# Kernel optimization log

Measured on AMD Instinct MI355X. Metric: run time of the kernel, lower is better.

## Reference

```python
import jax, jax.numpy as jnp
import numpy as np

B, C, H, W = 8, 48, 256, 256
N_PROMPTS = 16
N_EXPERTS = 8
N_GROUPS = 4
TOP_K = 2
GROUP_DIM = C // N_GROUPS
DN = ('NCHW', 'OIHW', 'NCHW')


def _conv(x, w, groups=1, pad=0):
    return jax.lax.conv_general_dilated(
        x, w, window_strides=(1, 1), padding=[(pad, pad), (pad, pad)],
        dimension_numbers=DN, feature_group_count=groups)


def setup_inputs() -> dict:
    key = jax.random.key(0)
    ks = jax.random.split(key, 10)
    s = 0.02
    return {
        'x': jax.random.normal(ks[0], (B, C, H, W), jnp.float32),
        'P_hat': jax.random.normal(ks[1], (B, N_PROMPTS, C), jnp.float32),
        'proj_a_w': jax.random.normal(ks[2], (C, C, 1, 1), jnp.float32) * s,
        'proj_b_w': jax.random.normal(ks[3], (C, C, 1, 1), jnp.float32) * s,
        'dw_b_w': jax.random.normal(ks[4], (C, 1, 3, 3), jnp.float32) * s,
        'fi_align_w': jax.random.normal(ks[5], (C, N_GROUPS, 1, 1), jnp.float32) * s,
        'expert_w1': jax.random.normal(ks[6], (N_EXPERTS, C, C, 3, 3), jnp.float32) * s,
        'expert_w2': jax.random.normal(ks[7], (N_EXPERTS, C, C, 3, 3), jnp.float32) * s,
        'router_w': jax.random.normal(ks[8], (N_EXPERTS, C), jnp.float32) * s,
        'router_b': jax.random.normal(ks[9], (N_EXPERTS,), jnp.float32) * s,
    }


def reference(x, P_hat, proj_a_w, proj_b_w, dw_b_w, fi_align_w,
              expert_w1, expert_w2, router_w, router_b):
    b, c, h, w = x.shape
    # branch a: 1x1 proj + group-wise prompt-conditioned filter activation
    xa = _conv(x, proj_a_w)                               # [B,C,H,W]
    p_avg = P_hat.mean(axis=1)                            # [B,C]
    xa_g = xa.reshape(b, N_GROUPS, GROUP_DIM, h * w)      # [B,G,gd,HW]
    p_g = p_avg.reshape(b, N_GROUPS, GROUP_DIM)           # [B,G,gd]
    fi = jnp.einsum('bgc,bgcn->bgn', p_g, xa_g)           # [B,G,HW]
    fi = fi.reshape(b, N_GROUPS, h, w)
    fi = _conv(fi, fi_align_w)                            # [B,C,H,W]
    # branch b: 1x1 proj + depthwise 3x3
    xb = _conv(_conv(x, proj_b_w), dw_b_w, groups=c, pad=1)
    Fx = xb + fi
    # routing: GAP -> linear -> top-k softmax gate
    gap = Fx.mean(axis=(2, 3))                            # [B,C]
    scores = gap @ router_w.T + router_b                  # [B,E]
    topk_val, topk_idx = jax.lax.top_k(scores, TOP_K)
    gate = jnp.zeros_like(scores).at[
        jnp.arange(b)[:, None], topk_idx
    ].set(jax.nn.softmax(topk_val, axis=-1))              # [B,E]
    # experts: dense compute then weighted sum (matches dense-then-mask math)
    out = jnp.zeros_like(Fx)
    for i in range(N_EXPERTS):
        hmid = jax.nn.gelu(_conv(Fx, expert_w1[i], pad=1), approximate=False)
        e_out = _conv(hmid, expert_w2[i], pad=1)
        out = out + gate[:, i][:, None, None, None] * e_out
    return out + x
```

## Files before the change

### kernel.cpp

```cpp
#include <hip/hip_runtime.h>
#include <hip/hip_bf16.h>
#include <math.h>

#define BATCH 8
#define CH 48
#define HH 256
#define WW 256
#define NPROMPT 16
#define NEXP 8
#define NGRP 4
#define GDIM 12
#define HW (HH * WW)

#define FRAG_ELEMS (9 * 3 * 2 * 64 * 8)
#define FRAG_BYTES (FRAG_ELEMS * 2)

typedef short bf16x8 __attribute__((ext_vector_type(8)));
typedef float f32x4  __attribute__((ext_vector_type(4)));
typedef unsigned short u16x4 __attribute__((ext_vector_type(4)));

#define TILE_W 16
#define TILE_H 8
#define ITILE_W 18
#define ITILE_H 10
#define NPIX (ITILE_W * ITILE_H)
#define PIXB 128
#define ROWB (ITILE_W * PIXB)
#define STAGE_K 23
#define LDSBYTES (STAGE_K * 1024)
#define GPIXB 96
#define IMGB ((size_t)HW * GPIXB)
#define NTILES 512

__device__ __forceinline__ unsigned short f2bf(float f) {
    unsigned u = __float_as_uint(f);
    unsigned r = (u + 0x7FFFu + ((u >> 16) & 1u)) >> 16;
    return (unsigned short)r;
}

__device__ __forceinline__ void load_lds16(const void* g, void* l) {
    __builtin_amdgcn_global_load_lds(
        (const __attribute__((address_space(1))) unsigned int*)g,
        (__attribute__((address_space(3))) unsigned int*)l, 16, 0, 0);
}

__global__ __launch_bounds__(256) void precompute_kernel(
    const float* __restrict__ P_hat,
    const float* __restrict__ proj_a_w,
    const float* __restrict__ proj_b_w,
    const float* __restrict__ dw_b_w,
    const float* __restrict__ fi_align_w,
    unsigned short* __restrict__ wfxf,
    float* __restrict__ zpage)
{
    int b = blockIdx.x;
    int tid = threadIdx.x;
    __shared__ float p_avg[CH];
    __shared__ float W_fi[NGRP * CH];
    __shared__ float W_a[CH * CH];

    if (tid < CH) {
        float s = 0.f;
        for (int n = 0; n < NPROMPT; n++)
            s += P_hat[(b * NPROMPT + n) * CH + tid];
        p_avg[tid] = s * (1.0f / NPROMPT);
    }
    if (b == 0 && tid < 64) zpage[tid] = 0.f;
    __syncthreads();

    if (tid < NGRP * CH) {
        int g = tid / CH, k = tid % CH;
        float s = 0.f;
        for (int j = 0; j < GDIM; j++) {
            int c = g * GDIM + j;
            s += p_avg[c] * proj_a_w[c * CH + k];
        }
        W_fi[tid] = s;
    }
    __syncthreads();

    for (int e = tid; e < CH * CH; e += 256) {
        int o = e / CH, k = e % CH;
        float s = 0.f;
        for (int g = 0; g < NGRP; g++)
            s += fi_align_w[o * NGRP + g] * W_fi[g * CH + k];
        W_a[e] = s;
    }
    __syncthreads();

    for (int i = tid; i < FRAG_ELEMS; i += 256) {
        int j = i & 7;
        int lane = (i >> 3) & 63;
        int blk = i >> 9;
        int kb = blk & 1;
        int tmp = blk >> 1;
        int mt = tmp % 3, tap = tmp / 3;
        int oc = mt * 16 + (lane & 15);
        int cin = kb * 32 + (lane >> 4) * 8 + j;
        float v = 0.f;
        if (cin < CH) {
            v = dw_b_w[oc * 9 + tap] * proj_b_w[oc * CH + cin];
            if (tap == 4) v += W_a[oc * CH + cin];
        }
        wfxf[(size_t)b * FRAG_ELEMS + i] = f2bf(v);
    }
}

__global__ __launch_bounds__(256) void repack_kernel(
    const float* __restrict__ w1, const float* __restrict__ w2,
    unsigned short* __restrict__ w1f, unsigned short* __restrict__ w2f)
{
    int e = blockIdx.x;
    const float* src = blockIdx.y ? w2 : w1;
    unsigned short* dst = blockIdx.y ? w2f : w1f;
    for (int i = threadIdx.x; i < FRAG_ELEMS; i += 256) {
        int j = i & 7;
        int lane = (i >> 3) & 63;
        int blk = i >> 9;
        int kb = blk & 1;
        int tmp = blk >> 1;
        int mt = tmp % 3, tap = tmp / 3;
        int oc = mt * 16 + (lane & 15);
        int cin = kb * 32 + (lane >> 4) * 8 + j;
        float v = (cin < CH) ? src[(((size_t)e * CH + oc) * CH + cin) * 9 + tap] : 0.f;
        dst[(size_t)e * FRAG_ELEMS + i] = f2bf(v);
    }
}

__global__ __launch_bounds__(256) void transpose_kernel(
    const float* __restrict__ x, unsigned short* __restrict__ xT)
{
    __shared__ float t[CH * 65];
    int pix0 = blockIdx.x * 64;
    int b = pix0 >> 16;
    int rem = pix0 & 65535;
    int tid = threadIdx.x;
    int px = tid & 63, c0 = tid >> 6;

    float v[12];
#pragma unroll
    for (int k = 0; k < 12; k++)
        v[k] = x[(((size_t)(b * CH + c0 + 4 * k)) << 16) + rem + px];
#pragma unroll
    for (int k = 0; k < 12; k++)
        t[(c0 + 4 * k) * 65 + px] = v[k];
    __syncthreads();

#pragma unroll
    for (int k = 0; k < 2; k++) {
        int w = tid + 256 * k;
        if (w < 384) {
            int p2 = w / 6, o = w % 6;
            bf16x8 pk;
#pragma unroll
            for (int j = 0; j < 8; j++)
                pk[j] = (short)f2bf(t[(o * 8 + j) * 65 + p2]);
            *(bf16x8*)((char*)xT + (size_t)pix0 * GPIXB + (size_t)w * 16) = pk;
        }
    }
}

__device__ __forceinline__ void stage_swz(
    const char* __restrict__ srcimg, int oy0, int ox0,
    char* smem, const char* __restrict__ zp)
{
    int wv = threadIdx.x >> 6, lane = threadIdx.x & 63;
    for (int k = wv; k < STAGE_K; k += 4) {
        int w = k * 64 + lane;
        int px = w >> 3, o = w & 7;
        int yy = px / ITILE_W, xx = px - yy * ITILE_W;
        int gy = oy0 + yy - 1, gx = ox0 + xx - 1;
        int m = o ^ (gx & 7);
        const char* g = zp;
        if (px < NPIX && (unsigned)gy < 256u && (unsigned)gx < 256u && m < 6)
            g = srcimg + (size_t)((gy << 8) + gx) * GPIXB + m * 16;
        load_lds16(g, smem + k * 1024);
    }
}

template <bool ACC, bool SWAP>
__device__ __forceinline__ void conv_core(
    const char* smem, const unsigned short* __restrict__ wfrag,
    int ox0, f32x4 acc[2][3])
{
    const int lane = threadIdx.x & 63;
    const int wv = threadIdx.x >> 6;
    const int n = lane & 15;
    const int quad = lane >> 4;
    const bf16x8* wp = (const bf16x8*)wfrag;

    if (!ACC) {
#pragma unroll
        for (int g = 0; g < 2; ++g)
#pragma unroll
            for (int mt = 0; mt < 3; ++mt)
                acc[g][mt] = (f32x4){0.f, 0.f, 0.f, 0.f};
    }

    int colb0[3], colb1[3];
#pragma unroll
    for (int dx = 0; dx < 3; ++dx) {
        int key = (ox0 - 1 + dx + n) & 7;
        colb0[dx] = (dx + n) * PIXB + ((quad ^ key) * 16);
        colb1[dx] = (dx + n) * PIXB + (((quad + 4) ^ key) * 16);
    }

    bf16x8 a[2][6];
#pragma unroll
    for (int mt = 0; mt < 3; ++mt) {
        a[0][mt]     = wp[(mt * 2 + 0) * 64 + lane];
        a[0][mt + 3] = wp[(mt * 2 + 1) * 64 + lane];
    }

#pragma unroll
    for (int tap = 0; tap < 9; ++tap) {
        const int cur = tap & 1;
        if (tap < 8) {
#pragma unroll
            for (int mt = 0; mt < 3; ++mt) {
                a[cur ^ 1][mt]     = wp[(((tap + 1) * 3 + mt) * 2 + 0) * 64 + lane];
                a[cur ^ 1][mt + 3] = wp[(((tap + 1) * 3 + mt) * 2 + 1) * 64 + lane];
            }
        }
        const int dy = tap / 3, dx = tap % 3;
#pragma unroll
        for (int g = 0; g < 2; ++g) {
            const int rowb = (wv * 2 + g + dy) * ROWB;
            bf16x8 b0 = *(const bf16x8*)(smem + rowb + colb0[dx]);
            bf16x8 b1 = *(const bf16x8*)(smem + rowb + colb1[dx]);
            if (SWAP) {
                acc[g][0] = __builtin_amdgcn_mfma_f32_16x16x32_bf16(b0, a[cur][0], acc[g][0], 0, 0, 0);
                acc[g][1] = __builtin_amdgcn_mfma_f32_16x16x32_bf16(b0, a[cur][1], acc[g][1], 0, 0, 0);
                acc[g][2] = __builtin_amdgcn_mfma_f32_16x16x32_bf16(b0, a[cur][2], acc[g][2], 0, 0, 0);
                acc[g][0] = __builtin_amdgcn_mfma_f32_16x16x32_bf16(b1, a[cur][3], acc[g][0], 0, 0, 0);
                acc[g][1] = __builtin_amdgcn_mfma_f32_16x16x32_bf16(b1, a[cur][4], acc[g][1], 0, 0, 0);
                acc[g][2] = __builtin_amdgcn_mfma_f32_16x16x32_bf16(b1, a[cur][5], acc[g][2], 0, 0, 0);
            } else {
                acc[g][0] = __builtin_amdgcn_mfma_f32_16x16x32_bf16(a[cur][0], b0, acc[g][0], 0, 0, 0);
                acc[g][1] = __builtin_amdgcn_mfma_f32_16x16x32_bf16(a[cur][1], b0, acc[g][1], 0, 0, 0);
                acc[g][2] = __builtin_amdgcn_mfma_f32_16x16x32_bf16(a[cur][2], b0, acc[g][2], 0, 0, 0);
                acc[g][0] = __builtin_amdgcn_mfma_f32_16x16x32_bf16(a[cur][3], b1, acc[g][0], 0, 0, 0);
                acc[g][1] = __builtin_amdgcn_mfma_f32_16x16x32_bf16(a[cur][4], b1, acc[g][1], 0, 0, 0);
                acc[g][2] = __builtin_amdgcn_mfma_f32_16x16x32_bf16(a[cur][5], b1, acc[g][2], 0, 0, 0);
            }
        }
    }
}

__device__ __forceinline__ void store_pix(
    char* __restrict__ dstimg, int row, int col, int quad,
    const f32x4 v[3])
{
    size_t pb = (size_t)((row << 8) + col) * GPIXB;
#pragma unroll
    for (int mt = 0; mt < 3; ++mt) {
        u16x4 pk;
#pragma unroll
        for (int r = 0; r < 4; ++r) pk[r] = f2bf(v[mt][r]);
        *(u16x4*)(dstimg + pb + mt * 32 + quad * 8) = pk;
    }
}

__global__ __launch_bounds__(256, 4) void fxconv_kernel(
    const unsigned short* __restrict__ xT, const unsigned short* __restrict__ wfxf,
    unsigned short* __restrict__ Fx, float* __restrict__ gapP,
    const float* __restrict__ zp)
{
    __shared__ __align__(16) char smem[LDSBYTES];
    int ox0 = blockIdx.x * TILE_W, oy0 = blockIdx.y * TILE_H, b = blockIdx.z;

    stage_swz((const char*)xT + (size_t)b * IMGB, oy0, ox0, smem, (const char*)zp);
    __syncthreads();

    f32x4 acc[2][3];
    conv_core<false, false>(smem, wfxf + (size_t)b * FRAG_ELEMS, ox0, acc);

    const int lane = threadIdx.x & 63;
    const int wv = threadIdx.x >> 6;
    const int n = lane & 15, quad = lane >> 4;
    char* dimg = (char*)Fx + (size_t)b * IMGB;

    float gsum[3][4];
#pragma unroll
    for (int mt = 0; mt < 3; ++mt)
#pragma unroll
        for (int r = 0; r < 4; ++r) gsum[mt][r] = 0.f;

#pragma unroll
    for (int g = 0; g < 2; ++g) {
        int row = oy0 + wv * 2 + g;
        store_pix(dimg, row, ox0 + n, quad, acc[g]);
#pragma unroll
        for (int mt = 0; mt < 3; ++mt)
#pragma unroll
            for (int r = 0; r < 4; ++r) gsum[mt][r] += acc[g][mt][r];
    }
#pragma unroll
    for (int mt = 0; mt < 3; ++mt)
#pragma unroll
        for (int r = 0; r < 4; ++r) {
            float v = gsum[mt][r];
            v += __shfl_xor(v, 1);
            v += __shfl_xor(v, 2);
            v += __shfl_xor(v, 4);
            v += __shfl_xor(v, 8);
            gsum[mt][r] = v;
        }

    __syncthreads();
    float* smemf = (float*)smem;
    if (n == 0) {
#pragma unroll
        for (int mt = 0; mt < 3; ++mt)
#pragma unroll
            for (int r = 0; r < 4; ++r)
                smemf[wv * CH + mt * 16 + quad * 4 + r] = gsum[mt][r];
    }
    __syncthreads();
    int t = threadIdx.x;
    if (t < CH) {
        float v = smemf[t] + smemf[CH + t] + smemf[2 * CH + t] + smemf[3 * CH + t];
        int tile = blockIdx.y * 16 + blockIdx.x;
        gapP[((size_t)b * NTILES + tile) * CH + t] = v;
    }
}

__global__ __launch_bounds__(256) void route_kernel(
    const float* __restrict__ gapP,
    const float* __restrict__ router_w,
    const float* __restrict__ router_b,
    float* __restrict__ gate, int* __restrict__ eidx)
{
    __shared__ float red4[4 * CH];
    __shared__ float scs[NEXP];
    int b = blockIdx.x, t = threadIdx.x;
    int lane = t & 63, wv = t >> 6;

    const float* s1 = gapP + ((size_t)b * NTILES + t) * CH;
    const float* s2 = s1 + 256 * CH;
    float s[CH];
#pragma unroll
    for (int c = 0; c < CH; c++) s[c] = s1[c] + s2[c];
#pragma unroll
    for (int c = 0; c < CH; c++) {
        float v = s[c];
        v += __shfl_xor(v, 1);
        v += __shfl_xor(v, 2);
        v += __shfl_xor(v, 4);
        v += __shfl_xor(v, 8);
        v += __shfl_xor(v, 16);
        v += __shfl_xor(v, 32);
        if (lane == 0) red4[wv * CH + c] = v;
    }
    __syncthreads();

    if (t < NEXP) {
        float sc = router_b[t];
        for (int c = 0; c < CH; c++) {
            float g = (red4[c] + red4[CH + c] + red4[2 * CH + c] + red4[3 * CH + c])
                      * (1.0f / HW);
            sc += g * router_w[t * CH + c];
        }
        scs[t] = sc;
    }
    __syncthreads();

    if (t == 0) {
        float v0 = -1e30f, v1 = -1e30f;
        int i0 = 0, i1 = 0;
        for (int e = 0; e < NEXP; e++) {
            float se = scs[e];
            if (se > v0) { v1 = v0; i1 = i0; v0 = se; i0 = e; }
            else if (se > v1) { v1 = se; i1 = e; }
        }
        float ex = expf(v1 - v0);
        float dn = 1.0f / (1.0f + ex);
        gate[b * 2 + 0] = dn;
        gate[b * 2 + 1] = ex * dn;
        eidx[b * 2 + 0] = i0;
        eidx[b * 2 + 1] = i1;
    }
}

__global__ __launch_bounds__(256) void scale_kernel(
    const unsigned short* __restrict__ w2f, const float* __restrict__ gate,
    const int* __restrict__ eidx, unsigned short* __restrict__ w2s)
{
    int b = blockIdx.x, s = blockIdx.y;
    int e = eidx[b * 2 + s];
    float g = gate[b * 2 + s];
    const unsigned short* src = w2f + (size_t)e * FRAG_ELEMS;
    unsigned short* dst = w2s + (size_t)(b * 2 + s) * FRAG_ELEMS;
    for (int i = threadIdx.x; i < FRAG_ELEMS; i += 256) {
        float v = __uint_as_float((unsigned)src[i] << 16);
        dst[i] = f2bf(v * g);
    }
}

__global__ __launch_bounds__(256, 4) void conv1_both_kernel(
    const unsigned short* __restrict__ Fx, const unsigned short* __restrict__ w1f,
    const int* __restrict__ eidx, const float* __restrict__ zp,
    unsigned short* __restrict__ hmid0, unsigned short* __restrict__ hmid1)
{
    __shared__ __align__(16) char smem[LDSBYTES];
    int ox0 = blockIdx.x * TILE_W, oy0 = blockIdx.y * TILE_H, b = blockIdx.z;

    stage_swz((const char*)Fx + (size_t)b * IMGB, oy0, ox0, smem, (const char*)zp);
    __syncthreads();

    const int lane = threadIdx.x & 63;
    const int wv = threadIdx.x >> 6;
    const int n = lane & 15, quad = lane >> 4;

    f32x4 acc[2][3];
#pragma unroll
    for (int s = 0; s < 2; ++s) {
        int e = __builtin_amdgcn_readfirstlane(eidx[b * 2 + s]);
        conv_core<false, false>(smem, w1f + (size_t)e * FRAG_ELEMS, ox0, acc);
        char* dimg = (char*)(s ? hmid1 : hmid0) + (size_t)b * IMGB;
#pragma unroll
        for (int g = 0; g < 2; ++g) {
            int row = oy0 + wv * 2 + g;
            f32x4 h[3];
#pragma unroll
            for (int mt = 0; mt < 3; ++mt)
#pragma unroll
                for (int r = 0; r < 4; ++r) {
                    float a = acc[g][mt][r];
                    h[mt][r] = 0.5f * a * (1.0f + erff(a * 0.70710678118654752f));
                }
            store_pix(dimg, row, ox0 + n, quad, h);
        }
    }
}

__global__ __launch_bounds__(256, 4) void conv2_both_kernel(
    const unsigned short* __restrict__ hmid0, const unsigned short* __restrict__ hmid1,
    const unsigned short* __restrict__ w2s, const float* __restrict__ zp,
    const float* __restrict__ x, float* __restrict__ out)
{
    __shared__ __align__(16) char smem[LDSBYTES];
    int d = blockIdx.x;
    int k8   = d & 7;
    int half = (d >> 3) & 1;
    int rest = d >> 4;
    int bx = k8 * 2 + half;
    int by = rest & 31;
    int b  = rest >> 5;
    int ox0 = bx * TILE_W, oy0 = by * TILE_H;

    const int lane = threadIdx.x & 63;
    const int wv = threadIdx.x >> 6;
    const int n = lane & 15, quad = lane >> 4;

    f32x4 xr[2][3];
#pragma unroll
    for (int g = 0; g < 2; ++g) {
        int row = oy0 + wv * 2 + g;
#pragma unroll
        for (int nt = 0; nt < 3; ++nt) {
            int oc = nt * 16 + n;
            size_t idx = (((size_t)b * CH + oc) << 16) + (row << 8) + ox0 + quad * 4;
            xr[g][nt] = *(const f32x4*)(x + idx);
        }
    }

    f32x4 acc[2][3];

    stage_swz((const char*)hmid0 + (size_t)b * IMGB, oy0, ox0, smem, (const char*)zp);
    __syncthreads();
    conv_core<false, true>(smem, w2s + (size_t)(b * 2 + 0) * FRAG_ELEMS, ox0, acc);
    __syncthreads();

    stage_swz((const char*)hmid1 + (size_t)b * IMGB, oy0, ox0, smem, (const char*)zp);
    __syncthreads();
    conv_core<true, true>(smem, w2s + (size_t)(b * 2 + 1) * FRAG_ELEMS, ox0, acc);

#pragma unroll
    for (int g = 0; g < 2; ++g) {
        int row = oy0 + wv * 2 + g;
#pragma unroll
        for (int nt = 0; nt < 3; ++nt) {
            int oc = nt * 16 + n;
            size_t idx = (((size_t)b * CH + oc) << 16) + (row << 8) + ox0 + quad * 4;
            *(f32x4*)(out + idx) = xr[g][nt] + acc[g][nt];
        }
    }
}

extern "C" void kernel_launch(void* const* d_in, const int* in_sizes, int n_in,
                              void* d_out, int out_size, void* d_ws, size_t ws_size,
                              hipStream_t stream) {
    (void)in_sizes; (void)n_in; (void)out_size; (void)ws_size;
    const float* x          = (const float*)d_in[0];
    const float* P_hat      = (const float*)d_in[1];
    const float* proj_a_w   = (const float*)d_in[2];
    const float* proj_b_w   = (const float*)d_in[3];
    const float* dw_b_w     = (const float*)d_in[4];
    const float* fi_align_w = (const float*)d_in[5];
    const float* expert_w1  = (const float*)d_in[6];
    const float* expert_w2  = (const float*)d_in[7];
    const float* router_w   = (const float*)d_in[8];
    const float* router_b   = (const float*)d_in[9];
    float* out = (float*)d_out;

    char* ob = (char*)d_out;
    unsigned short* Fx   = (unsigned short*)ob;
    unsigned short* wfxf = (unsigned short*)(ob + 62914560);
    unsigned short* w1f  = (unsigned short*)(ob + 62914560 + FRAG_BYTES * NEXP);
    unsigned short* w2f  = (unsigned short*)(ob + 62914560 + 2 * FRAG_BYTES * NEXP);
    float*          gapP = (float*)(ob + 64241664);

    char* ws = (char*)d_ws;
    unsigned short* xT    = (unsigned short*)ws;
    unsigned short* hmid1 = (unsigned short*)ws;
    unsigned short* hmid0 = (unsigned short*)(ws + 50331648);
    unsigned short* w2s   = (unsigned short*)(ws + 100663296);
    float* zp   = (float*)(ws + 100663296 + 884736);
    float* gate = (float*)(ws + 100663296 + 884736 + 256 + 1536);
    int*   eidx = (int*)(gate + BATCH * 2);

    precompute_kernel<<<dim3(BATCH), 256, 0, stream>>>(
        P_hat, proj_a_w, proj_b_w, dw_b_w, fi_align_w, wfxf, zp);

    repack_kernel<<<dim3(NEXP, 2), 256, 0, stream>>>(
        expert_w1, expert_w2, w1f, w2f);

    transpose_kernel<<<dim3(BATCH * HW / 64), 256, 0, stream>>>(x, xT);

    fxconv_kernel<<<dim3(16, 32, BATCH), 256, 0, stream>>>(xT, wfxf, Fx, gapP, zp);

    route_kernel<<<dim3(BATCH), 256, 0, stream>>>(gapP, router_w, router_b, gate, eidx);

    scale_kernel<<<dim3(BATCH, 2), 256, 0, stream>>>(w2f, gate, eidx, w2s);

    conv1_both_kernel<<<dim3(16, 32, BATCH), 256, 0, stream>>>(
        Fx, w1f, eidx, zp, hmid0, hmid1);

    conv2_both_kernel<<<dim3(4096), 256, 0, stream>>>(
        hmid0, hmid1, w2s, zp, x, out);
}
```

Measured before the change: 569.5 us.

## Stage conv outputs through LDS for coalesced stores; drop weight double-buffering

The fxconv and conv1 kernels now write their bf16 outputs into an LDS tile buffer, then stream the whole tile to global memory as contiguous 16-byte chunks, replacing the scattered 8-byte per-lane stores. The weight-fragment loads in conv_core are no longer double-buffered across taps, and conv2 loads the residual x after the convolutions instead of before. These changes lower register pressure and improve store coalescing, at the cost of extra LDS (which may reduce occupancy), extra barriers, and exposed latency on the weight and x loads.

Measured after the change: 471.4 us. 17.2% less time.

```diff
diff --git a/kernel.cpp b/kernel.cpp
--- a/kernel.cpp
+++ b/kernel.cpp
@@ -28,6 +28,7 @@
 #define ROWB (ITILE_W * PIXB)
 #define STAGE_K 23
 #define LDSBYTES (STAGE_K * 1024)
+#define RBUFB (TILE_H * TILE_W * GPIXB)
 #define GPIXB 96
 #define IMGB ((size_t)HW * GPIXB)
 #define NTILES 512
@@ -205,22 +206,13 @@
         colb1[dx] = (dx + n) * PIXB + (((quad + 4) ^ key) * 16);
     }
 
-    bf16x8 a[2][6];
-#pragma unroll
-    for (int mt = 0; mt < 3; ++mt) {
-        a[0][mt]     = wp[(mt * 2 + 0) * 64 + lane];
-        a[0][mt + 3] = wp[(mt * 2 + 1) * 64 + lane];
-    }
-
 #pragma unroll
     for (int tap = 0; tap < 9; ++tap) {
-        const int cur = tap & 1;
-        if (tap < 8) {
-#pragma unroll
-            for (int mt = 0; mt < 3; ++mt) {
-                a[cur ^ 1][mt]     = wp[(((tap + 1) * 3 + mt) * 2 + 0) * 64 + lane];
-                a[cur ^ 1][mt + 3] = wp[(((tap + 1) * 3 + mt) * 2 + 1) * 64 + lane];
-            }
+        bf16x8 a[6];
+#pragma unroll
+        for (int mt = 0; mt < 3; ++mt) {
+            a[mt]     = wp[((tap * 3 + mt) * 2 + 0) * 64 + lane];
+            a[mt + 3] = wp[((tap * 3 + mt) * 2 + 1) * 64 + lane];
         }
         const int dy = tap / 3, dx = tap % 3;
 #pragma unroll
@@ -229,35 +221,47 @@
             bf16x8 b0 = *(const bf16x8*)(smem + rowb + colb0[dx]);
             bf16x8 b1 = *(const bf16x8*)(smem + rowb + colb1[dx]);
             if (SWAP) {
-                acc[g][0] = __builtin_amdgcn_mfma_f32_16x16x32_bf16(b0, a[cur][0], acc[g][0], 0, 0, 0);
-                acc[g][1] = __builtin_amdgcn_mfma_f32_16x16x32_bf16(b0, a[cur][1], acc[g][1], 0, 0, 0);
-                acc[g][2] = __builtin_amdgcn_mfma_f32_16x16x32_bf16(b0, a[cur][2], acc[g][2], 0, 0, 0);
-                acc[g][0] = __builtin_amdgcn_mfma_f32_16x16x32_bf16(b1, a[cur][3], acc[g][0], 0, 0, 0);
-                acc[g][1] = __builtin_amdgcn_mfma_f32_16x16x32_bf16(b1, a[cur][4], acc[g][1], 0, 0, 0);
-                acc[g][2] = __builtin_amdgcn_mfma_f32_16x16x32_bf16(b1, a[cur][5], acc[g][2], 0, 0, 0);
+                acc[g][0] = __builtin_amdgcn_mfma_f32_16x16x32_bf16(b0, a[0], acc[g][0], 0, 0, 0);
+                acc[g][1] = __builtin_amdgcn_mfma_f32_16x16x32_bf16(b0, a[1], acc[g][1], 0, 0, 0);
+                acc[g][2] = __builtin_amdgcn_mfma_f32_16x16x32_bf16(b0, a[2], acc[g][2], 0, 0, 0);
+                acc[g][0] = __builtin_amdgcn_mfma_f32_16x16x32_bf16(b1, a[3], acc[g][0], 0, 0, 0);
+                acc[g][1] = __builtin_amdgcn_mfma_f32_16x16x32_bf16(b1, a[4], acc[g][1], 0, 0, 0);
+                acc[g][2] = __builtin_amdgcn_mfma_f32_16x16x32_bf16(b1, a[5], acc[g][2], 0, 0, 0);
             } else {
-                acc[g][0] = __builtin_amdgcn_mfma_f32_16x16x32_bf16(a[cur][0], b0, acc[g][0], 0, 0, 0);
-                acc[g][1] = __builtin_amdgcn_mfma_f32_16x16x32_bf16(a[cur][1], b0, acc[g][1], 0, 0, 0);
-                acc[g][2] = __builtin_amdgcn_mfma_f32_16x16x32_bf16(a[cur][2], b0, acc[g][2], 0, 0, 0);
-                acc[g][0] = __builtin_amdgcn_mfma_f32_16x16x32_bf16(a[cur][3], b1, acc[g][0], 0, 0, 0);
-                acc[g][1] = __builtin_amdgcn_mfma_f32_16x16x32_bf16(a[cur][4], b1, acc[g][1], 0, 0, 0);
-                acc[g][2] = __builtin_amdgcn_mfma_f32_16x16x32_bf16(a[cur][5], b1, acc[g][2], 0, 0, 0);
+                acc[g][0] = __builtin_amdgcn_mfma_f32_16x16x32_bf16(a[0], b0, acc[g][0], 0, 0, 0);
+                acc[g][1] = __builtin_amdgcn_mfma_f32_16x16x32_bf16(a[1], b0, acc[g][1], 0, 0, 0);
+                acc[g][2] = __builtin_amdgcn_mfma_f32_16x16x32_bf16(a[2], b0, acc[g][2], 0, 0, 0);
+                acc[g][0] = __builtin_amdgcn_mfma_f32_16x16x32_bf16(a[3], b1, acc[g][0], 0, 0, 0);
+                acc[g][1] = __builtin_amdgcn_mfma_f32_16x16x32_bf16(a[4], b1, acc[g][1], 0, 0, 0);
+                acc[g][2] = __builtin_amdgcn_mfma_f32_16x16x32_bf16(a[5], b1, acc[g][2], 0, 0, 0);
             }
         }
     }
 }
 
-__device__ __forceinline__ void store_pix(
-    char* __restrict__ dstimg, int row, int col, int quad,
-    const f32x4 v[3])
-{
-    size_t pb = (size_t)((row << 8) + col) * GPIXB;
+__device__ __forceinline__ void pack_rbuf(
+    char* rbuf, int prow, int n, int quad, const f32x4 v[3])
+{
 #pragma unroll
     for (int mt = 0; mt < 3; ++mt) {
         u16x4 pk;
 #pragma unroll
         for (int r = 0; r < 4; ++r) pk[r] = f2bf(v[mt][r]);
-        *(u16x4*)(dstimg + pb + mt * 32 + quad * 8) = pk;
+        *(u16x4*)(rbuf + (prow * TILE_W + n) * GPIXB + mt * 32 + quad * 8) = pk;
+    }
+}
+
+__device__ __forceinline__ void stream_rbuf(
+    const char* rbuf, char* __restrict__ dimg, int oy0, int ox0)
+{
+    int t = threadIdx.x;
+#pragma unroll
+    for (int i = 0; i < 3; ++i) {
+        int c = t + i * 256;
+        int row = c / 96;
+        int off = (c - row * 96) * 16;
+        bf16x8 v = *(const bf16x8*)(rbuf + c * 16);
+        *(bf16x8*)(dimg + (size_t)(((oy0 + row) << 8) + ox0) * GPIXB + off) = v;
     }
 }
 
@@ -267,6 +271,7 @@
     const float* __restrict__ zp)
 {
     __shared__ __align__(16) char smem[LDSBYTES];
+    __shared__ __align__(16) char rbuf[RBUFB];
     int ox0 = blockIdx.x * TILE_W, oy0 = blockIdx.y * TILE_H, b = blockIdx.z;
 
     stage_swz((const char*)xT + (size_t)b * IMGB, oy0, ox0, smem, (const char*)zp);
@@ -278,7 +283,6 @@
     const int lane = threadIdx.x & 63;
     const int wv = threadIdx.x >> 6;
     const int n = lane & 15, quad = lane >> 4;
-    char* dimg = (char*)Fx + (size_t)b * IMGB;
 
     float gsum[3][4];
 #pragma unroll
@@ -288,8 +292,7 @@
 
 #pragma unroll
     for (int g = 0; g < 2; ++g) {
-        int row = oy0 + wv * 2 + g;
-        store_pix(dimg, row, ox0 + n, quad, acc[g]);
+        pack_rbuf(rbuf, wv * 2 + g, n, quad, acc[g]);
 #pragma unroll
         for (int mt = 0; mt < 3; ++mt)
 #pragma unroll
@@ -308,6 +311,9 @@
         }
 
     __syncthreads();
+
+    stream_rbuf(rbuf, (char*)Fx + (size_t)b * IMGB, oy0, ox0);
+
     float* smemf = (float*)smem;
     if (n == 0) {
 #pragma unroll
@@ -403,6 +409,7 @@
     unsigned short* __restrict__ hmid0, unsigned short* __restrict__ hmid1)
 {
     __shared__ __align__(16) char smem[LDSBYTES];
+    __shared__ __align__(16) char rbuf[RBUFB];
     int ox0 = blockIdx.x * TILE_W, oy0 = blockIdx.y * TILE_H, b = blockIdx.z;
 
     stage_swz((const char*)Fx + (size_t)b * IMGB, oy0, ox0, smem, (const char*)zp);
@@ -417,10 +424,8 @@
     for (int s = 0; s < 2; ++s) {
         int e = __builtin_amdgcn_readfirstlane(eidx[b * 2 + s]);
         conv_core<false, false>(smem, w1f + (size_t)e * FRAG_ELEMS, ox0, acc);
-        char* dimg = (char*)(s ? hmid1 : hmid0) + (size_t)b * IMGB;
 #pragma unroll
         for (int g = 0; g < 2; ++g) {
-            int row = oy0 + wv * 2 + g;
             f32x4 h[3];
 #pragma unroll
             for (int mt = 0; mt < 3; ++mt)
@@ -429,8 +434,11 @@
                     float a = acc[g][mt][r];
                     h[mt][r] = 0.5f * a * (1.0f + erff(a * 0.70710678118654752f));
                 }
-            store_pix(dimg, row, ox0 + n, quad, h);
-        }
+            pack_rbuf(rbuf, wv * 2 + g, n, quad, h);
+        }
+        __syncthreads();
+        stream_rbuf(rbuf, (char*)(s ? hmid1 : hmid0) + (size_t)b * IMGB, oy0, ox0);
+        __syncthreads();
     }
 }
 
@@ -453,7 +461,17 @@
     const int wv = threadIdx.x >> 6;
     const int n = lane & 15, quad = lane >> 4;
 
-    f32x4 xr[2][3];
+    f32x4 acc[2][3];
+
+    stage_swz((const char*)hmid0 + (size_t)b * IMGB, oy0, ox0, smem, (const char*)zp);
+    __syncthreads();
+    conv_core<false, true>(smem, w2s + (size_t)(b * 2 + 0) * FRAG_ELEMS, ox0, acc);
+    __syncthreads();
+
+    stage_swz((const char*)hmid1 + (size_t)b * IMGB, oy0, ox0, smem, (const char*)zp);
+    __syncthreads();
+    conv_core<true, true>(smem, w2s + (size_t)(b * 2 + 1) * FRAG_ELEMS, ox0, acc);
+
 #pragma unroll
     for (int g = 0; g < 2; ++g) {
         int row = oy0 + wv * 2 + g;
@@ -461,29 +479,8 @@
         for (int nt = 0; nt < 3; ++nt) {
             int oc = nt * 16 + n;
             size_t idx = (((size_t)b * CH + oc) << 16) + (row << 8) + ox0 + quad * 4;
-            xr[g][nt] = *(const f32x4*)(x + idx);
-        }
-    }
-
-    f32x4 acc[2][3];
-
-    stage_swz((const char*)hmid0 + (size_t)b * IMGB, oy0, ox0, smem, (const char*)zp);
-    __syncthreads();
-    conv_core<false, true>(smem, w2s + (size_t)(b * 2 + 0) * FRAG_ELEMS, ox0, acc);
-    __syncthreads();
-
-    stage_swz((const char*)hmid1 + (size_t)b * IMGB, oy0, ox0, smem, (const char*)zp);
-    __syncthreads();
-    conv_core<true, true>(smem, w2s + (size_t)(b * 2 + 1) * FRAG_ELEMS, ox0, acc);
-
-#pragma unroll
-    for (int g = 0; g < 2; ++g) {
-        int row = oy0 + wv * 2 + g;
-#pragma unroll
-        for (int nt = 0; nt < 3; ++nt) {
-            int oc = nt * 16 + n;
-            size_t idx = (((size_t)b * CH + oc) << 16) + (row << 8) + ox0 + quad * 4;
-            *(f32x4*)(out + idx) = xr[g][nt] + acc[g][nt];
+            f32x4 xr = *(const f32x4*)(x + idx);
+            *(f32x4*)(out + idx) = xr + acc[g][nt];
         }
     }
 }
```
